# Performance work log

Measured on AMD Instinct MI355X. Metric: run time of the kernel, lower is better.

Reference implementation:

```python
import jax, jax.numpy as jnp
import numpy as np

# Vanilla tanh-RNN (num_layers=1, batch_first) followed by tanh + dropout(eval: identity) + linear.

def setup_inputs() -> dict:
    key = jax.random.key(0)
    ks = jax.random.split(key, 7)
    B, T, I, H, C = 16384, 64, 64, 100, 40
    s_ih = 1.0 / np.sqrt(H)
    return {
        "x": jax.random.normal(ks[0], (B, T * I), dtype=jnp.float32),
        "W_ih": jax.random.normal(ks[1], (H, I), dtype=jnp.float32) * s_ih,
        "W_hh": jax.random.normal(ks[2], (H, H), dtype=jnp.float32) * s_ih,
        "b_ih": jax.random.normal(ks[3], (H,), dtype=jnp.float32) * s_ih,
        "b_hh": jax.random.normal(ks[4], (H,), dtype=jnp.float32) * s_ih,
        "fc_W": jax.random.normal(ks[5], (C, H), dtype=jnp.float32) * 0.1,
        "fc_b": jax.random.normal(ks[6], (C,), dtype=jnp.float32) * 0.1,
    }


def reference(x, W_ih, W_hh, b_ih, b_hh, fc_W, fc_b):
    B = x.shape[0]
    x = x.reshape(B, 64, 64)  # [B, T, I]
    # Precompute input projections for all steps in one GEMM: [B, T, H]
    xp = jnp.einsum("bti,hi->bth", x, W_ih) + b_ih + b_hh
    h0 = jnp.zeros((B, W_hh.shape[0]), dtype=x.dtype)

    def step(h, xp_t):  # h: [B, H], xp_t: [B, H]
        h_new = jnp.tanh(xp_t + h @ W_hh.T)
        return h_new, None

    h_last, _ = jax.lax.scan(step, h0, jnp.swapaxes(xp, 0, 1))  # scan over T
    out = jnp.tanh(h_last)  # tanh on last-step output
    # dropout(p=0.2) in eval mode = identity
    return out @ fc_W.T + fc_b  # [B, 40]
```

## Files before the change

### kernel.cpp

```cpp
#include <hip/hip_runtime.h>


typedef _Float16 half8 __attribute__((ext_vector_type(8)));
typedef float float4_t __attribute__((ext_vector_type(4)));
typedef unsigned int uint4_t __attribute__((ext_vector_type(4)));

#define ROW_BYTES 1088
#define BUF_BYTES (16 * ROW_BYTES)
#define GLOAD16(gp, lp)                                                   \
  __builtin_amdgcn_global_load_lds(                                       \
      (const __attribute__((address_space(1))) void*)(gp),                \
      (__attribute__((address_space(3))) void*)(lp), 16, 0, 0)

__device__ __forceinline__ float tanh_fast(float x) {
  float e = __builtin_amdgcn_exp2f(x * 2.8853900817779268f);
  return 1.0f - 2.0f * __builtin_amdgcn_rcpf(e + 1.0f);
}

__device__ __forceinline__ unsigned int pk2(float lo, float hi) {
  return __builtin_bit_cast(unsigned int, __builtin_amdgcn_cvt_pkrtz(lo, hi));
}

__device__ __forceinline__ half8 pack4(unsigned int a, unsigned int b,
                                       unsigned int c, unsigned int d) {
  uint4_t u = {a, b, c, d};
  return __builtin_bit_cast(half8, u);
}

__device__ __forceinline__ void issue_slab(const float* srcl, int slab, char* buf) {
  const float* s = srcl + slab * 256;
  #pragma unroll
  for (int j = 0; j < 16; ++j) {
    GLOAD16(s, buf + j * ROW_BYTES);
    s += 4096;
  }
}

__global__ __launch_bounds__(64, 1) void rnn_fused(
    const float* __restrict__ x, const float* __restrict__ W_ih,
    const float* __restrict__ W_hh, const float* __restrict__ b_ih,
    const float* __restrict__ b_hh, const float* __restrict__ fc_W,
    const float* __restrict__ fc_b, float* __restrict__ out, int B)
{
  __shared__ char xring[2 * BUF_BYTES];
  const int lane = threadIdx.x & 63;
  const int g = lane >> 4;
  const int c = lane & 15;
  const int rowbase = blockIdx.x * 16;

  half8 wih[2][7];
  half8 whh[4][7];
  float4_t bias[7];

  #pragma unroll
  for (int nt = 0; nt < 7; ++nt) {
    int nb = nt * 16 + 4 * g;
    float4_t bi = {0.f, 0.f, 0.f, 0.f};
    if (nb + 3 < 100) {
      float4_t a = *(const float4_t*)(b_ih + nb);
      float4_t b = *(const float4_t*)(b_hh + nb);
      bi = a + b;
    }
    bias[nt] = bi;

    int nrow = nt * 16 + c;
    bool rv = (nrow < 100);
    #pragma unroll
    for (int kb = 0; kb < 2; ++kb) {
      float4_t f0 = {0.f,0.f,0.f,0.f}, f1 = {0.f,0.f,0.f,0.f};
      if (rv) {
        const float* p = W_ih + nrow * 64 + kb * 32 + g * 8;
        f0 = *(const float4_t*)p;
        f1 = *(const float4_t*)(p + 4);
      }
      half8 h;
      #pragma unroll
      for (int j = 0; j < 4; ++j) {
        h[2 * j]     = (_Float16)f0[j];
        h[2 * j + 1] = (_Float16)f1[j];
      }
      wih[kb][nt] = h;
    }
    #pragma unroll
    for (int kb = 0; kb < 4; ++kb) {
      int clo = kb * 32 + 4 * g;
      int chi = clo + 16;
      float4_t f0 = {0.f,0.f,0.f,0.f}, f1 = {0.f,0.f,0.f,0.f};
      if (rv && clo + 3 < 100) f0 = *(const float4_t*)(W_hh + nrow * 100 + clo);
      if (rv && chi + 3 < 100) f1 = *(const float4_t*)(W_hh + nrow * 100 + chi);
      half8 h;
      #pragma unroll
      for (int j = 0; j < 4; ++j) {
        h[2 * j]     = (_Float16)f0[j];
        h[2 * j + 1] = (_Float16)f1[j];
      }
      whh[kb][nt] = h;
    }
  }

  const float* srcl = x + (size_t)rowbase * 4096 + lane * 4;
  issue_slab(srcl, 0, xring);
  issue_slab(srcl, 1, xring + BUF_BYTES);

  const unsigned ring_base =
      (unsigned)(uintptr_t)(__attribute__((address_space(3))) char*)xring;
  const unsigned xa0 = ring_base + (unsigned)(c * ROW_BYTES + g * 32);

  float4_t acc[7];
  half8 hfrag[4];
  #pragma unroll
  for (int kb = 0; kb < 4; ++kb) hfrag[kb] = (half8)(_Float16)0.0f;

  for (int grp = 0; grp < 16; ++grp) {
    asm volatile("s_waitcnt vmcnt(16)" ::: "memory");
    unsigned xg = xa0 + (unsigned)((grp & 1) * BUF_BYTES);

    #pragma unroll
    for (int t4 = 0; t4 < 4; ++t4) {
      unsigned xs = xg + (unsigned)(t4 * 256);
      float4_t s0, s1, s2, s3;
      asm volatile(
          "ds_read_b128 %0, %4 offset:0\n\t"
          "ds_read_b128 %1, %4 offset:16\n\t"
          "ds_read_b128 %2, %4 offset:128\n\t"
          "ds_read_b128 %3, %4 offset:144"
          : "=&v"(s0), "=&v"(s1), "=&v"(s2), "=&v"(s3)
          : "v"(xs) : "memory");

      #pragma unroll
      for (int nt = 0; nt < 7; ++nt)
        acc[nt] = __builtin_amdgcn_mfma_f32_16x16x32_f16(whh[0][nt], hfrag[0], bias[nt], 0, 0, 0);
      #pragma unroll
      for (int kb = 1; kb < 4; ++kb)
        #pragma unroll
        for (int nt = 0; nt < 7; ++nt)
          acc[nt] = __builtin_amdgcn_mfma_f32_16x16x32_f16(whh[kb][nt], hfrag[kb], acc[nt], 0, 0, 0);

      asm volatile("s_waitcnt lgkmcnt(0)"
                   : "+v"(s0), "+v"(s1), "+v"(s2), "+v"(s3) :: "memory");
      __builtin_amdgcn_sched_barrier(0);

      half8 xb0 = pack4(pk2(s0[0], s1[0]), pk2(s0[1], s1[1]),
                        pk2(s0[2], s1[2]), pk2(s0[3], s1[3]));
      half8 xb1 = pack4(pk2(s2[0], s3[0]), pk2(s2[1], s3[1]),
                        pk2(s2[2], s3[2]), pk2(s2[3], s3[3]));
      #pragma unroll
      for (int nt = 0; nt < 7; ++nt) {
        acc[nt] = __builtin_amdgcn_mfma_f32_16x16x32_f16(wih[0][nt], xb0, acc[nt], 0, 0, 0);
        acc[nt] = __builtin_amdgcn_mfma_f32_16x16x32_f16(wih[1][nt], xb1, acc[nt], 0, 0, 0);
      }

      #pragma unroll
      for (int nt = 0; nt < 7; ++nt)
        #pragma unroll
        for (int v = 0; v < 4; ++v)
          acc[nt][v] = tanh_fast(acc[nt][v]);

      #pragma unroll
      for (int kb = 0; kb < 3; ++kb)
        hfrag[kb] = pack4(pk2(acc[2*kb][0], acc[2*kb+1][0]),
                          pk2(acc[2*kb][1], acc[2*kb+1][1]),
                          pk2(acc[2*kb][2], acc[2*kb+1][2]),
                          pk2(acc[2*kb][3], acc[2*kb+1][3]));
      hfrag[3] = pack4(pk2(acc[6][0], 0.0f), pk2(acc[6][1], 0.0f),
                       pk2(acc[6][2], 0.0f), pk2(acc[6][3], 0.0f));
    }

    int sl = grp + 2; if (sl > 15) sl = 15;
    issue_slab(srcl, sl, xring + (grp & 1) * BUF_BYTES);
  }

  #pragma unroll
  for (int nt = 0; nt < 7; ++nt)
    #pragma unroll
    for (int v = 0; v < 4; ++v)
      acc[nt][v] = tanh_fast(acc[nt][v]);

  half8 zf[4];
  #pragma unroll
  for (int kb = 0; kb < 3; ++kb)
    zf[kb] = pack4(pk2(acc[2*kb][0], acc[2*kb+1][0]),
                   pk2(acc[2*kb][1], acc[2*kb+1][1]),
                   pk2(acc[2*kb][2], acc[2*kb+1][2]),
                   pk2(acc[2*kb][3], acc[2*kb+1][3]));
  zf[3] = pack4(pk2(acc[6][0], 0.0f), pk2(acc[6][1], 0.0f),
                pk2(acc[6][2], 0.0f), pk2(acc[6][3], 0.0f));

  half8 wfc[4][3];
  float4_t bfc[3];
  #pragma unroll
  for (int nt = 0; nt < 3; ++nt) {
    int nb = nt * 16 + 4 * g;
    float4_t bi = {0.f,0.f,0.f,0.f};
    if (nb + 3 < 40) bi = *(const float4_t*)(fc_b + nb);
    bfc[nt] = bi;

    int nrow = nt * 16 + c;
    bool rv = (nrow < 40);
    #pragma unroll
    for (int kb = 0; kb < 4; ++kb) {
      int clo = kb * 32 + 4 * g;
      int chi = clo + 16;
      float4_t f0 = {0.f,0.f,0.f,0.f}, f1 = {0.f,0.f,0.f,0.f};
      if (rv && clo + 3 < 100) f0 = *(const float4_t*)(fc_W + nrow * 100 + clo);
      if (rv && chi + 3 < 100) f1 = *(const float4_t*)(fc_W + nrow * 100 + chi);
      half8 h;
      #pragma unroll
      for (int j = 0; j < 4; ++j) {
        h[2 * j]     = (_Float16)f0[j];
        h[2 * j + 1] = (_Float16)f1[j];
      }
      wfc[kb][nt] = h;
    }
  }

  float4_t oacc[3];
  #pragma unroll
  for (int nt = 0; nt < 3; ++nt) oacc[nt] = bfc[nt];
  #pragma unroll
  for (int kb = 0; kb < 4; ++kb)
    #pragma unroll
    for (int nt = 0; nt < 3; ++nt)
      oacc[nt] = __builtin_amdgcn_mfma_f32_16x16x32_f16(wfc[kb][nt], zf[kb], oacc[nt], 0, 0, 0);

  #pragma unroll
  for (int nt = 0; nt < 3; ++nt)
    #pragma unroll
    for (int v = 0; v < 4; ++v) {
      int n = nt * 16 + 4 * g + v;
      if (n < 40)
        out[(size_t)(rowbase + c) * 40 + n] = oacc[nt][v];
    }
}

extern "C" void kernel_launch(void* const* d_in, const int* in_sizes, int n_in,
                              void* d_out, int out_size, void* d_ws, size_t ws_size,
                              hipStream_t stream) {
  const float* x    = (const float*)d_in[0];
  const float* W_ih = (const float*)d_in[1];
  const float* W_hh = (const float*)d_in[2];
  const float* b_ih = (const float*)d_in[3];
  const float* b_hh = (const float*)d_in[4];
  const float* fc_W = (const float*)d_in[5];
  const float* fc_b = (const float*)d_in[6];
  float* outp = (float*)d_out;

  int B = in_sizes[0] / 4096;
  int grid = (B + 15) / 16;
  rnn_fused<<<grid, 64, 0, stream>>>(x, W_ih, W_hh, b_ih, b_hh, fc_W, fc_b, outp, B);
}
```

Before: 65.88 us.

## Software-pipeline RNN recurrence: precompute input projection ahead, interleave tanh with MFMA

Restructures the recurrent loop so the input projection for step t+1 (W_ih·x plus bias) is computed one step ahead into a separate accumulator. The tanh and pack of each hidden chunk is interleaved with the W_hh MFMAs that consume it, which shortens the serial dependency chain per timestep. The x slab prefetch now starts before the weights are loaded, the slab refill is issued mid-group after an explicit vmcnt(0) wait, and LDS reads are issued two steps ahead. In exchange it needs more accumulator registers and a changed wait/ring-buffer schedule, which could introduce hazards.

```diff
diff --git a/kernel.cpp b/kernel.cpp
--- a/kernel.cpp
+++ b/kernel.cpp
@@ -33,6 +33,82 @@
   for (int j = 0; j < 16; ++j) {
     GLOAD16(s, buf + j * ROW_BYTES);
     s += 4096;
+  }
+}
+
+template <int T4>
+__device__ __forceinline__ void rnn_step(
+    float4_t (&cur)[7], float4_t (&nxt)[7], float4_t (&xacc)[7],
+    const half8 (&whh)[4][7], const half8 (&wih)[2][7],
+    const float4_t (&bias)[7], unsigned xa0, int i)
+{
+  int ft = i + 2; if (ft > 63) ft = 63;
+  unsigned xs = xa0 + (unsigned)(((ft >> 2) & 1) * BUF_BYTES)
+                    + (unsigned)((ft & 3) * 256);
+  if (T4 == 2) asm volatile("s_waitcnt vmcnt(0)" ::: "memory");
+  float4_t s0, s1, s2, s3;
+  asm volatile(
+      "ds_read_b128 %0, %4 offset:0\n\t"
+      "ds_read_b128 %1, %4 offset:16\n\t"
+      "ds_read_b128 %2, %4 offset:128\n\t"
+      "ds_read_b128 %3, %4 offset:144"
+      : "=&v"(s0), "=&v"(s1), "=&v"(s2), "=&v"(s3)
+      : "v"(xs) : "memory");
+
+  #pragma unroll
+  for (int v = 0; v < 4; ++v) {
+    cur[0][v] = tanh_fast(cur[0][v]);
+    cur[1][v] = tanh_fast(cur[1][v]);
+  }
+  half8 hf0 = pack4(pk2(cur[0][0], cur[1][0]), pk2(cur[0][1], cur[1][1]),
+                    pk2(cur[0][2], cur[1][2]), pk2(cur[0][3], cur[1][3]));
+  #pragma unroll
+  for (int nt = 0; nt < 7; ++nt)
+    nxt[nt] = __builtin_amdgcn_mfma_f32_16x16x32_f16(whh[0][nt], hf0, xacc[nt], 0, 0, 0);
+
+  #pragma unroll
+  for (int v = 0; v < 4; ++v) {
+    cur[2][v] = tanh_fast(cur[2][v]);
+    cur[3][v] = tanh_fast(cur[3][v]);
+  }
+  half8 hf1 = pack4(pk2(cur[2][0], cur[3][0]), pk2(cur[2][1], cur[3][1]),
+                    pk2(cur[2][2], cur[3][2]), pk2(cur[2][3], cur[3][3]));
+  #pragma unroll
+  for (int nt = 0; nt < 7; ++nt)
+    nxt[nt] = __builtin_amdgcn_mfma_f32_16x16x32_f16(whh[1][nt], hf1, nxt[nt], 0, 0, 0);
+
+  asm volatile("s_waitcnt lgkmcnt(0)"
+               : "+v"(s0), "+v"(s1), "+v"(s2), "+v"(s3) :: "memory");
+  __builtin_amdgcn_sched_barrier(0);
+  half8 xb0 = pack4(pk2(s0[0], s1[0]), pk2(s0[1], s1[1]),
+                    pk2(s0[2], s1[2]), pk2(s0[3], s1[3]));
+  half8 xb1 = pack4(pk2(s2[0], s3[0]), pk2(s2[1], s3[1]),
+                    pk2(s2[2], s3[2]), pk2(s2[3], s3[3]));
+
+  #pragma unroll
+  for (int v = 0; v < 4; ++v) {
+    cur[4][v] = tanh_fast(cur[4][v]);
+    cur[5][v] = tanh_fast(cur[5][v]);
+  }
+  half8 hf2 = pack4(pk2(cur[4][0], cur[5][0]), pk2(cur[4][1], cur[5][1]),
+                    pk2(cur[4][2], cur[5][2]), pk2(cur[4][3], cur[5][3]));
+  #pragma unroll
+  for (int nt = 0; nt < 7; ++nt)
+    nxt[nt] = __builtin_amdgcn_mfma_f32_16x16x32_f16(whh[2][nt], hf2, nxt[nt], 0, 0, 0);
+
+  #pragma unroll
+  for (int v = 0; v < 4; ++v)
+    cur[6][v] = tanh_fast(cur[6][v]);
+  half8 hf3 = pack4(pk2(cur[6][0], 0.0f), pk2(cur[6][1], 0.0f),
+                    pk2(cur[6][2], 0.0f), pk2(cur[6][3], 0.0f));
+  #pragma unroll
+  for (int nt = 0; nt < 7; ++nt)
+    nxt[nt] = __builtin_amdgcn_mfma_f32_16x16x32_f16(whh[3][nt], hf3, nxt[nt], 0, 0, 0);
+
+  #pragma unroll
+  for (int nt = 0; nt < 7; ++nt) {
+    float4_t tmp = __builtin_amdgcn_mfma_f32_16x16x32_f16(wih[0][nt], xb0, bias[nt], 0, 0, 0);
+    xacc[nt]     = __builtin_amdgcn_mfma_f32_16x16x32_f16(wih[1][nt], xb1, tmp, 0, 0, 0);
   }
 }
 
@@ -47,6 +123,10 @@
   const int g = lane >> 4;
   const int c = lane & 15;
   const int rowbase = blockIdx.x * 16;
+
+  const float* srcl = x + (size_t)rowbase * 4096 + lane * 4;
+  issue_slab(srcl, 0, xring);
+  issue_slab(srcl, 1, xring + BUF_BYTES);
 
   half8 wih[2][7];
   half8 whh[4][7];
@@ -98,93 +178,65 @@
     }
   }
 
-  const float* srcl = x + (size_t)rowbase * 4096 + lane * 4;
-  issue_slab(srcl, 0, xring);
-  issue_slab(srcl, 1, xring + BUF_BYTES);
-
   const unsigned ring_base =
       (unsigned)(uintptr_t)(__attribute__((address_space(3))) char*)xring;
   const unsigned xa0 = ring_base + (unsigned)(c * ROW_BYTES + g * 32);
 
-  float4_t acc[7];
-  half8 hfrag[4];
-  #pragma unroll
-  for (int kb = 0; kb < 4; ++kb) hfrag[kb] = (half8)(_Float16)0.0f;
+  float4_t acc[7], nacc[7], xacc[7];
+
+  asm volatile("s_waitcnt vmcnt(16)" ::: "memory");
+  #pragma unroll
+  for (int f = 0; f < 2; ++f) {
+    unsigned xs = xa0 + (unsigned)(f * 256);
+    float4_t s0, s1, s2, s3;
+    asm volatile(
+        "ds_read_b128 %0, %4 offset:0\n\t"
+        "ds_read_b128 %1, %4 offset:16\n\t"
+        "ds_read_b128 %2, %4 offset:128\n\t"
+        "ds_read_b128 %3, %4 offset:144\n\t"
+        "s_waitcnt lgkmcnt(0)"
+        : "=&v"(s0), "=&v"(s1), "=&v"(s2), "=&v"(s3)
+        : "v"(xs) : "memory");
+    __builtin_amdgcn_sched_barrier(0);
+    half8 xb0 = pack4(pk2(s0[0], s1[0]), pk2(s0[1], s1[1]),
+                      pk2(s0[2], s1[2]), pk2(s0[3], s1[3]));
+    half8 xb1 = pack4(pk2(s2[0], s3[0]), pk2(s2[1], s3[1]),
+                      pk2(s2[2], s3[2]), pk2(s2[3], s3[3]));
+    #pragma unroll
+    for (int nt = 0; nt < 7; ++nt) {
+      float4_t tmp = __builtin_amdgcn_mfma_f32_16x16x32_f16(wih[0][nt], xb0, bias[nt], 0, 0, 0);
+      if (f == 0) acc[nt]  = __builtin_amdgcn_mfma_f32_16x16x32_f16(wih[1][nt], xb1, tmp, 0, 0, 0);
+      else        xacc[nt] = __builtin_amdgcn_mfma_f32_16x16x32_f16(wih[1][nt], xb1, tmp, 0, 0, 0);
+    }
+  }
 
   for (int grp = 0; grp < 16; ++grp) {
-    asm volatile("s_waitcnt vmcnt(16)" ::: "memory");
-    unsigned xg = xa0 + (unsigned)((grp & 1) * BUF_BYTES);
-
-    #pragma unroll
-    for (int t4 = 0; t4 < 4; ++t4) {
-      unsigned xs = xg + (unsigned)(t4 * 256);
-      float4_t s0, s1, s2, s3;
-      asm volatile(
-          "ds_read_b128 %0, %4 offset:0\n\t"
-          "ds_read_b128 %1, %4 offset:16\n\t"
-          "ds_read_b128 %2, %4 offset:128\n\t"
-          "ds_read_b128 %3, %4 offset:144"
-          : "=&v"(s0), "=&v"(s1), "=&v"(s2), "=&v"(s3)
-          : "v"(xs) : "memory");
-
-      #pragma unroll
-      for (int nt = 0; nt < 7; ++nt)
-        acc[nt] = __builtin_amdgcn_mfma_f32_16x16x32_f16(whh[0][nt], hfrag[0], bias[nt], 0, 0, 0);
-      #pragma unroll
-      for (int kb = 1; kb < 4; ++kb)
-        #pragma unroll
-        for (int nt = 0; nt < 7; ++nt)
-          acc[nt] = __builtin_amdgcn_mfma_f32_16x16x32_f16(whh[kb][nt], hfrag[kb], acc[nt], 0, 0, 0);
-
-      asm volatile("s_waitcnt lgkmcnt(0)"
-                   : "+v"(s0), "+v"(s1), "+v"(s2), "+v"(s3) :: "memory");
-      __builtin_amdgcn_sched_barrier(0);
-
-      half8 xb0 = pack4(pk2(s0[0], s1[0]), pk2(s0[1], s1[1]),
-                        pk2(s0[2], s1[2]), pk2(s0[3], s1[3]));
-      half8 xb1 = pack4(pk2(s2[0], s3[0]), pk2(s2[1], s3[1]),
-                        pk2(s2[2], s3[2]), pk2(s2[3], s3[3]));
-      #pragma unroll
-      for (int nt = 0; nt < 7; ++nt) {
-        acc[nt] = __builtin_amdgcn_mfma_f32_16x16x32_f16(wih[0][nt], xb0, acc[nt], 0, 0, 0);
-        acc[nt] = __builtin_amdgcn_mfma_f32_16x16x32_f16(wih[1][nt], xb1, acc[nt], 0, 0, 0);
-      }
-
-      #pragma unroll
-      for (int nt = 0; nt < 7; ++nt)
-        #pragma unroll
-        for (int v = 0; v < 4; ++v)
-          acc[nt][v] = tanh_fast(acc[nt][v]);
-
-      #pragma unroll
-      for (int kb = 0; kb < 3; ++kb)
-        hfrag[kb] = pack4(pk2(acc[2*kb][0], acc[2*kb+1][0]),
-                          pk2(acc[2*kb][1], acc[2*kb+1][1]),
-                          pk2(acc[2*kb][2], acc[2*kb+1][2]),
-                          pk2(acc[2*kb][3], acc[2*kb+1][3]));
-      hfrag[3] = pack4(pk2(acc[6][0], 0.0f), pk2(acc[6][1], 0.0f),
-                       pk2(acc[6][2], 0.0f), pk2(acc[6][3], 0.0f));
-    }
-
-    int sl = grp + 2; if (sl > 15) sl = 15;
-    issue_slab(srcl, sl, xring + (grp & 1) * BUF_BYTES);
+    int i0 = grp * 4;
+    rnn_step<0>(acc,  nacc, xacc, whh, wih, bias, xa0, i0);
+    rnn_step<1>(nacc, acc,  xacc, whh, wih, bias, xa0, i0 + 1);
+    rnn_step<2>(acc,  nacc, xacc, whh, wih, bias, xa0, i0 + 2);
+    {
+      int sl = grp + 2; if (sl > 15) sl = 15;
+      issue_slab(srcl, sl, xring + (grp & 1) * BUF_BYTES);
+    }
+    rnn_step<3>(nacc, acc,  xacc, whh, wih, bias, xa0, i0 + 3);
   }
 
   #pragma unroll
   for (int nt = 0; nt < 7; ++nt)
     #pragma unroll
     for (int v = 0; v < 4; ++v)
-      acc[nt][v] = tanh_fast(acc[nt][v]);
+      nacc[nt][v] = tanh_fast(nacc[nt][v]);
 
   half8 zf[4];
   #pragma unroll
   for (int kb = 0; kb < 3; ++kb)
-    zf[kb] = pack4(pk2(acc[2*kb][0], acc[2*kb+1][0]),
-                   pk2(acc[2*kb][1], acc[2*kb+1][1]),
-                   pk2(acc[2*kb][2], acc[2*kb+1][2]),
-                   pk2(acc[2*kb][3], acc[2*kb+1][3]));
-  zf[3] = pack4(pk2(acc[6][0], 0.0f), pk2(acc[6][1], 0.0f),
-                pk2(acc[6][2], 0.0f), pk2(acc[6][3], 0.0f));
+    zf[kb] = pack4(pk2(nacc[2*kb][0], nacc[2*kb+1][0]),
+                   pk2(nacc[2*kb][1], nacc[2*kb+1][1]),
+                   pk2(nacc[2*kb][2], nacc[2*kb+1][2]),
+                   pk2(nacc[2*kb][3], nacc[2*kb+1][3]));
+  zf[3] = pack4(pk2(nacc[6][0], 0.0f), pk2(nacc[6][1], 0.0f),
+                pk2(nacc[6][2], 0.0f), pk2(nacc[6][3], 0.0f));
 
   half8 wfc[4][3];
   float4_t bfc[3];
```

New measurement: 68.03 us. 3.3% more time.

## Split RNN hidden dimension across four cooperating waves with LDS exchange

Applied to the files above, without the earlier changes.

Each block now runs four waves instead of one, and each wave owns a slice of the hidden-unit tiles (2,2,2,1 tiles of 16). The slices are shared every timestep by writing the wave's packed h fragment to LDS and reading the others back, with an s_barrier per step. The x loads and the final FC are split across the waves the same way. The aim is to shorten the per-block serial MFMA chain and raise the number of waves per CU. In exchange it adds two barriers and LDS round-trips to every one of the 64 sequential steps, plus a larger LDS footprint per block.

```diff
diff --git a/kernel.cpp b/kernel.cpp
--- a/kernel.cpp
+++ b/kernel.cpp
@@ -7,6 +7,9 @@
 
 #define ROW_BYTES 1088
 #define BUF_BYTES (16 * ROW_BYTES)
+#define RING_BYTES (2 * BUF_BYTES)
+#define LDS_TOTAL (RING_BYTES + 4096)
+
 #define GLOAD16(gp, lp)                                                   \
   __builtin_amdgcn_global_load_lds(                                       \
       (const __attribute__((address_space(1))) void*)(gp),                \
@@ -16,44 +19,42 @@
   float e = __builtin_amdgcn_exp2f(x * 2.8853900817779268f);
   return 1.0f - 2.0f * __builtin_amdgcn_rcpf(e + 1.0f);
 }
-
 __device__ __forceinline__ unsigned int pk2(float lo, float hi) {
   return __builtin_bit_cast(unsigned int, __builtin_amdgcn_cvt_pkrtz(lo, hi));
 }
-
 __device__ __forceinline__ half8 pack4(unsigned int a, unsigned int b,
                                        unsigned int c, unsigned int d) {
   uint4_t u = {a, b, c, d};
   return __builtin_bit_cast(half8, u);
 }
 
-__device__ __forceinline__ void issue_slab(const float* srcl, int slab, char* buf) {
-  const float* s = srcl + slab * 256;
-  #pragma unroll
-  for (int j = 0; j < 16; ++j) {
-    GLOAD16(s, buf + j * ROW_BYTES);
-    s += 4096;
-  }
-}
-
-__global__ __launch_bounds__(64, 1) void rnn_fused(
+template <int R, int NTN>
+__device__ __forceinline__ void run_role(
     const float* __restrict__ x, const float* __restrict__ W_ih,
     const float* __restrict__ W_hh, const float* __restrict__ b_ih,
     const float* __restrict__ b_hh, const float* __restrict__ fc_W,
-    const float* __restrict__ fc_b, float* __restrict__ out, int B)
+    const float* __restrict__ fc_b, float* __restrict__ out,
+    int rowbase, int lane, char* lds)
 {
-  __shared__ char xring[2 * BUF_BYTES];
-  const int lane = threadIdx.x & 63;
   const int g = lane >> 4;
   const int c = lane & 15;
-  const int rowbase = blockIdx.x * 16;
-
-  half8 wih[2][7];
-  half8 whh[4][7];
-  float4_t bias[7];
-
+
+  const float* dsrc = x + (size_t)(rowbase + 4 * R) * 4096 + lane * 4;
+  {
+    #pragma unroll
+    for (int s = 0; s < 2; ++s)
+      #pragma unroll
+      for (int j = 0; j < 4; ++j)
+        GLOAD16(dsrc + j * 4096 + s * 256,
+                lds + s * BUF_BYTES + (4 * R + j) * ROW_BYTES);
+  }
+
+  half8 whh[4][NTN];
+  half8 wih[2][NTN];
+  float4_t bias[NTN];
   #pragma unroll
-  for (int nt = 0; nt < 7; ++nt) {
+  for (int nl = 0; nl < NTN; ++nl) {
+    int nt = 2 * R + nl;
     int nb = nt * 16 + 4 * g;
     float4_t bi = {0.f, 0.f, 0.f, 0.f};
     if (nb + 3 < 100) {
@@ -61,7 +62,7 @@
       float4_t b = *(const float4_t*)(b_hh + nb);
       bi = a + b;
     }
-    bias[nt] = bi;
+    bias[nl] = bi;
 
     int nrow = nt * 16 + c;
     bool rv = (nrow < 100);
@@ -75,11 +76,8 @@
       }
       half8 h;
       #pragma unroll
-      for (int j = 0; j < 4; ++j) {
-        h[2 * j]     = (_Float16)f0[j];
-        h[2 * j + 1] = (_Float16)f1[j];
-      }
-      wih[kb][nt] = h;
+      for (int j = 0; j < 4; ++j) { h[2*j] = (_Float16)f0[j]; h[2*j+1] = (_Float16)f1[j]; }
+      wih[kb][nl] = h;
     }
     #pragma unroll
     for (int kb = 0; kb < 4; ++kb) {
@@ -90,35 +88,32 @@
       if (rv && chi + 3 < 100) f1 = *(const float4_t*)(W_hh + nrow * 100 + chi);
       half8 h;
       #pragma unroll
-      for (int j = 0; j < 4; ++j) {
-        h[2 * j]     = (_Float16)f0[j];
-        h[2 * j + 1] = (_Float16)f1[j];
-      }
-      whh[kb][nt] = h;
-    }
-  }
-
-  const float* srcl = x + (size_t)rowbase * 4096 + lane * 4;
-  issue_slab(srcl, 0, xring);
-  issue_slab(srcl, 1, xring + BUF_BYTES);
-
-  const unsigned ring_base =
-      (unsigned)(uintptr_t)(__attribute__((address_space(3))) char*)xring;
-  const unsigned xa0 = ring_base + (unsigned)(c * ROW_BYTES + g * 32);
-
-  float4_t acc[7];
-  half8 hfrag[4];
-  #pragma unroll
-  for (int kb = 0; kb < 4; ++kb) hfrag[kb] = (half8)(_Float16)0.0f;
+      for (int j = 0; j < 4; ++j) { h[2*j] = (_Float16)f0[j]; h[2*j+1] = (_Float16)f1[j]; }
+      whh[kb][nl] = h;
+    }
+  }
+
+  const unsigned lbase =
+      (unsigned)(uintptr_t)(__attribute__((address_space(3))) char*)lds;
+  const unsigned xbase = lbase + (unsigned)(c * ROW_BYTES + g * 32);
+  const unsigned hbase = lbase + RING_BYTES + (unsigned)(c * 64 + g * 16);
+  const unsigned hw = hbase + R * 1024;
+
+  half8 own_hf = (half8)(_Float16)0.0f;
+  {
+    float4_t z = {0.f, 0.f, 0.f, 0.f};
+    asm volatile("ds_write_b128 %0, %1" :: "v"(hw), "v"(z) : "memory");
+  }
+  asm volatile("s_waitcnt vmcnt(4) lgkmcnt(0)\n\ts_barrier" ::: "memory");
+
+  float4_t acc[NTN];
 
   for (int grp = 0; grp < 16; ++grp) {
-    asm volatile("s_waitcnt vmcnt(16)" ::: "memory");
-    unsigned xg = xa0 + (unsigned)((grp & 1) * BUF_BYTES);
-
+    unsigned xg = xbase + (unsigned)((grp & 1) * BUF_BYTES);
     #pragma unroll
     for (int t4 = 0; t4 < 4; ++t4) {
       unsigned xs = xg + (unsigned)(t4 * 256);
-      float4_t s0, s1, s2, s3;
+      float4_t s0, s1, s2, s3, f0, f1, f2, f3;
       asm volatile(
           "ds_read_b128 %0, %4 offset:0\n\t"
           "ds_read_b128 %1, %4 offset:16\n\t"
@@ -126,111 +121,154 @@
           "ds_read_b128 %3, %4 offset:144"
           : "=&v"(s0), "=&v"(s1), "=&v"(s2), "=&v"(s3)
           : "v"(xs) : "memory");
-
-      #pragma unroll
-      for (int nt = 0; nt < 7; ++nt)
-        acc[nt] = __builtin_amdgcn_mfma_f32_16x16x32_f16(whh[0][nt], hfrag[0], bias[nt], 0, 0, 0);
-      #pragma unroll
-      for (int kb = 1; kb < 4; ++kb)
-        #pragma unroll
-        for (int nt = 0; nt < 7; ++nt)
-          acc[nt] = __builtin_amdgcn_mfma_f32_16x16x32_f16(whh[kb][nt], hfrag[kb], acc[nt], 0, 0, 0);
+      asm volatile(
+          "ds_read_b128 %0, %4 offset:0\n\t"
+          "ds_read_b128 %1, %4 offset:1024\n\t"
+          "ds_read_b128 %2, %4 offset:2048\n\t"
+          "ds_read_b128 %3, %4 offset:3072"
+          : "=&v"(f0), "=&v"(f1), "=&v"(f2), "=&v"(f3)
+          : "v"(hbase) : "memory");
+
+      #pragma unroll
+      for (int nl = 0; nl < NTN; ++nl)
+        acc[nl] = __builtin_amdgcn_mfma_f32_16x16x32_f16(whh[R][nl], own_hf, bias[nl], 0, 0, 0);
 
       asm volatile("s_waitcnt lgkmcnt(0)"
-                   : "+v"(s0), "+v"(s1), "+v"(s2), "+v"(s3) :: "memory");
+                   : "+v"(s0), "+v"(s1), "+v"(s2), "+v"(s3),
+                     "+v"(f0), "+v"(f1), "+v"(f2), "+v"(f3) :: "memory");
       __builtin_amdgcn_sched_barrier(0);
+
+      half8 hfr[4] = {__builtin_bit_cast(half8, f0), __builtin_bit_cast(half8, f1),
+                      __builtin_bit_cast(half8, f2), __builtin_bit_cast(half8, f3)};
+      #pragma unroll
+      for (int kb = 0; kb < 4; ++kb)
+        if (kb != R)
+          #pragma unroll
+          for (int nl = 0; nl < NTN; ++nl)
+            acc[nl] = __builtin_amdgcn_mfma_f32_16x16x32_f16(whh[kb][nl], hfr[kb], acc[nl], 0, 0, 0);
 
       half8 xb0 = pack4(pk2(s0[0], s1[0]), pk2(s0[1], s1[1]),
                         pk2(s0[2], s1[2]), pk2(s0[3], s1[3]));
       half8 xb1 = pack4(pk2(s2[0], s3[0]), pk2(s2[1], s3[1]),
                         pk2(s2[2], s3[2]), pk2(s2[3], s3[3]));
       #pragma unroll
-      for (int nt = 0; nt < 7; ++nt) {
-        acc[nt] = __builtin_amdgcn_mfma_f32_16x16x32_f16(wih[0][nt], xb0, acc[nt], 0, 0, 0);
-        acc[nt] = __builtin_amdgcn_mfma_f32_16x16x32_f16(wih[1][nt], xb1, acc[nt], 0, 0, 0);
-      }
-
-      #pragma unroll
-      for (int nt = 0; nt < 7; ++nt)
+      for (int nl = 0; nl < NTN; ++nl) {
+        acc[nl] = __builtin_amdgcn_mfma_f32_16x16x32_f16(wih[0][nl], xb0, acc[nl], 0, 0, 0);
+        acc[nl] = __builtin_amdgcn_mfma_f32_16x16x32_f16(wih[1][nl], xb1, acc[nl], 0, 0, 0);
+      }
+
+      #pragma unroll
+      for (int nl = 0; nl < NTN; ++nl)
         #pragma unroll
         for (int v = 0; v < 4; ++v)
-          acc[nt][v] = tanh_fast(acc[nt][v]);
-
-      #pragma unroll
-      for (int kb = 0; kb < 3; ++kb)
-        hfrag[kb] = pack4(pk2(acc[2*kb][0], acc[2*kb+1][0]),
-                          pk2(acc[2*kb][1], acc[2*kb+1][1]),
-                          pk2(acc[2*kb][2], acc[2*kb+1][2]),
-                          pk2(acc[2*kb][3], acc[2*kb+1][3]));
-      hfrag[3] = pack4(pk2(acc[6][0], 0.0f), pk2(acc[6][1], 0.0f),
-                       pk2(acc[6][2], 0.0f), pk2(acc[6][3], 0.0f));
-    }
-
-    int sl = grp + 2; if (sl > 15) sl = 15;
-    issue_slab(srcl, sl, xring + (grp & 1) * BUF_BYTES);
+          acc[nl][v] = tanh_fast(acc[nl][v]);
+      if (NTN == 2)
+        own_hf = pack4(pk2(acc[0][0], acc[1][0]), pk2(acc[0][1], acc[1][1]),
+                       pk2(acc[0][2], acc[1][2]), pk2(acc[0][3], acc[1][3]));
+      else
+        own_hf = pack4(pk2(acc[0][0], 0.0f), pk2(acc[0][1], 0.0f),
+                       pk2(acc[0][2], 0.0f), pk2(acc[0][3], 0.0f));
+
+      asm volatile("s_barrier" ::: "memory");
+      asm volatile("ds_write_b128 %0, %1"
+                   :: "v"(hw), "v"(__builtin_bit_cast(float4_t, own_hf)) : "memory");
+
+      if (t4 == 3) {
+        int sl = grp + 2; if (sl > 15) sl = 15;
+        #pragma unroll
+        for (int j = 0; j < 4; ++j)
+          GLOAD16(dsrc + j * 4096 + sl * 256,
+                  lds + (sl & 1) * BUF_BYTES + (4 * R + j) * ROW_BYTES);
+        asm volatile("s_waitcnt vmcnt(4) lgkmcnt(0)\n\ts_barrier" ::: "memory");
+      } else {
+        asm volatile("s_waitcnt lgkmcnt(0)\n\ts_barrier" ::: "memory");
+      }
+    }
   }
 
   #pragma unroll
-  for (int nt = 0; nt < 7; ++nt)
+  for (int nl = 0; nl < NTN; ++nl)
     #pragma unroll
     for (int v = 0; v < 4; ++v)
-      acc[nt][v] = tanh_fast(acc[nt][v]);
-
-  half8 zf[4];
-  #pragma unroll
-  for (int kb = 0; kb < 3; ++kb)
-    zf[kb] = pack4(pk2(acc[2*kb][0], acc[2*kb+1][0]),
-                   pk2(acc[2*kb][1], acc[2*kb+1][1]),
-                   pk2(acc[2*kb][2], acc[2*kb+1][2]),
-                   pk2(acc[2*kb][3], acc[2*kb+1][3]));
-  zf[3] = pack4(pk2(acc[6][0], 0.0f), pk2(acc[6][1], 0.0f),
-                pk2(acc[6][2], 0.0f), pk2(acc[6][3], 0.0f));
-
-  half8 wfc[4][3];
-  float4_t bfc[3];
-  #pragma unroll
-  for (int nt = 0; nt < 3; ++nt) {
-    int nb = nt * 16 + 4 * g;
-    float4_t bi = {0.f,0.f,0.f,0.f};
-    if (nb + 3 < 40) bi = *(const float4_t*)(fc_b + nb);
-    bfc[nt] = bi;
-
-    int nrow = nt * 16 + c;
-    bool rv = (nrow < 40);
-    #pragma unroll
-    for (int kb = 0; kb < 4; ++kb) {
-      int clo = kb * 32 + 4 * g;
-      int chi = clo + 16;
-      float4_t f0 = {0.f,0.f,0.f,0.f}, f1 = {0.f,0.f,0.f,0.f};
-      if (rv && clo + 3 < 100) f0 = *(const float4_t*)(fc_W + nrow * 100 + clo);
-      if (rv && chi + 3 < 100) f1 = *(const float4_t*)(fc_W + nrow * 100 + chi);
-      half8 h;
-      #pragma unroll
-      for (int j = 0; j < 4; ++j) {
-        h[2 * j]     = (_Float16)f0[j];
-        h[2 * j + 1] = (_Float16)f1[j];
-      }
-      wfc[kb][nt] = h;
-    }
-  }
-
-  float4_t oacc[3];
-  #pragma unroll
-  for (int nt = 0; nt < 3; ++nt) oacc[nt] = bfc[nt];
-  #pragma unroll
-  for (int kb = 0; kb < 4; ++kb)
-    #pragma unroll
-    for (int nt = 0; nt < 3; ++nt)
-      oacc[nt] = __builtin_amdgcn_mfma_f32_16x16x32_f16(wfc[kb][nt], zf[kb], oacc[nt], 0, 0, 0);
-
-  #pragma unroll
-  for (int nt = 0; nt < 3; ++nt)
+      acc[nl][v] = tanh_fast(acc[nl][v]);
+  half8 zf_own;
+  if (NTN == 2)
+    zf_own = pack4(pk2(acc[0][0], acc[1][0]), pk2(acc[0][1], acc[1][1]),
+                   pk2(acc[0][2], acc[1][2]), pk2(acc[0][3], acc[1][3]));
+  else
+    zf_own = pack4(pk2(acc[0][0], 0.0f), pk2(acc[0][1], 0.0f),
+                   pk2(acc[0][2], 0.0f), pk2(acc[0][3], 0.0f));
+  asm volatile("ds_write_b128 %0, %1"
+               :: "v"(hw), "v"(__builtin_bit_cast(float4_t, zf_own)) : "memory");
+  asm volatile("s_waitcnt lgkmcnt(0)\n\ts_barrier" ::: "memory");
+
+  if (R < 3) {
+    half8 wfc[4];
+    float4_t bfc = {0.f, 0.f, 0.f, 0.f};
+    {
+      int nb = R * 16 + 4 * g;
+      if (nb + 3 < 40) bfc = *(const float4_t*)(fc_b + nb);
+      int nrow = R * 16 + c;
+      bool rv = (nrow < 40);
+      #pragma unroll
+      for (int kb = 0; kb < 4; ++kb) {
+        int clo = kb * 32 + 4 * g;
+        int chi = clo + 16;
+        float4_t f0 = {0.f,0.f,0.f,0.f}, f1 = {0.f,0.f,0.f,0.f};
+        if (rv && clo + 3 < 100) f0 = *(const float4_t*)(fc_W + nrow * 100 + clo);
+        if (rv && chi + 3 < 100) f1 = *(const float4_t*)(fc_W + nrow * 100 + chi);
+        half8 h;
+        #pragma unroll
+        for (int j = 0; j < 4; ++j) { h[2*j] = (_Float16)f0[j]; h[2*j+1] = (_Float16)f1[j]; }
+        wfc[kb] = h;
+      }
+    }
+    float4_t z0, z1, z2, z3;
+    asm volatile(
+        "ds_read_b128 %0, %4 offset:0\n\t"
+        "ds_read_b128 %1, %4 offset:1024\n\t"
+        "ds_read_b128 %2, %4 offset:2048\n\t"
+        "ds_read_b128 %3, %4 offset:3072\n\t"
+        "s_waitcnt lgkmcnt(0)"
+        : "=&v"(z0), "=&v"(z1), "=&v"(z2), "=&v"(z3)
+        : "v"(hbase) : "memory");
+    __builtin_amdgcn_sched_barrier(0);
+    half8 zf[4] = {__builtin_bit_cast(half8, z0), __builtin_bit_cast(half8, z1),
+                   __builtin_bit_cast(half8, z2), __builtin_bit_cast(half8, z3)};
+    float4_t oacc = __builtin_amdgcn_mfma_f32_16x16x32_f16(wfc[0], zf[0], bfc, 0, 0, 0);
+    #pragma unroll
+    for (int kb = 1; kb < 4; ++kb)
+      oacc = __builtin_amdgcn_mfma_f32_16x16x32_f16(wfc[kb], zf[kb], oacc, 0, 0, 0);
+
     #pragma unroll
     for (int v = 0; v < 4; ++v) {
-      int n = nt * 16 + 4 * g + v;
+      int n = R * 16 + 4 * g + v;
       if (n < 40)
-        out[(size_t)(rowbase + c) * 40 + n] = oacc[nt][v];
-    }
+        out[(size_t)(rowbase + c) * 40 + n] = oacc[v];
+    }
+  }
+}
+
+__global__ __launch_bounds__(256, 4) void rnn_fused(
+    const float* __restrict__ x, const float* __restrict__ W_ih,
+    const float* __restrict__ W_hh, const float* __restrict__ b_ih,
+    const float* __restrict__ b_hh, const float* __restrict__ fc_W,
+    const float* __restrict__ fc_b, float* __restrict__ out, int B)
+{
+  __shared__ char lds[LDS_TOTAL];
+  const int lane = threadIdx.x & 63;
+  const int wave = threadIdx.x >> 6;
+  const int rowbase = blockIdx.x * 16;
+  if (rowbase >= B) return;
+
+  if (wave == 0)
+    run_role<0, 2>(x, W_ih, W_hh, b_ih, b_hh, fc_W, fc_b, out, rowbase, lane, lds);
+  else if (wave == 1)
+    run_role<1, 2>(x, W_ih, W_hh, b_ih, b_hh, fc_W, fc_b, out, rowbase, lane, lds);
+  else if (wave == 2)
+    run_role<2, 2>(x, W_ih, W_hh, b_ih, b_hh, fc_W, fc_b, out, rowbase, lane, lds);
+  else
+    run_role<3, 1>(x, W_ih, W_hh, b_ih, b_hh, fc_W, fc_b, out, rowbase, lane, lds);
 }
 
 extern "C" void kernel_launch(void* const* d_in, const int* in_sizes, int n_in,
@@ -247,5 +285,5 @@
 
   int B = in_sizes[0] / 4096;
   int grid = (B + 15) / 16;
-  rnn_fused<<<grid, 64, 0, stream>>>(x, W_ih, W_hh, b_ih, b_hh, fc_W, fc_b, outp, B);
-}
+  rnn_fused<<<grid, 256, 0, stream>>>(x, W_ih, W_hh, b_ih, b_hh, fc_W, fc_b, outp, B);
+}
```

Result: slower. 75.43 us (+14.5%).
